# Kernel optimization log

Hardware: AMD Instinct MI355X
Metric: run time of the kernel (lower is better)

The kernel has to match this reference:

```python
import jax, jax.numpy as jnp
import numpy as np

B, N, C = 16384, 4, 512
H = 8
HD = C // H
WIN = 2
SCALE = HD ** -0.5
HID = 2048


def _rel_pos_index(w):
    # same construction as the torch buffer, done in numpy (constant)
    coords = np.stack(np.meshgrid(np.arange(w), np.arange(w), indexing='ij'))  # [2,w,w]
    flat = coords.reshape(2, -1)                      # [2, w*w]
    rel = flat[:, :, None] - flat[:, None, :]         # [2, N, N]
    rel = rel.transpose(1, 2, 0).astype(np.int64)     # [N, N, 2]
    rel[:, :, 0] += w - 1
    rel[:, :, 1] += w - 1
    rel[:, :, 0] *= 2 * w - 1
    return rel.sum(-1)                                # [N, N]

REL_IDX = _rel_pos_index(WIN)


def setup_inputs() -> dict:
    key = jax.random.key(0)
    ks = jax.random.split(key, 8)
    s = lambda fan: 1.0 / np.sqrt(fan)
    return {
        'x': jax.random.normal(ks[0], (B, N, C), jnp.float32),
        'ln_g': jnp.ones((C,), jnp.float32),
        'ln_b': jnp.zeros((C,), jnp.float32),
        'qkv_w': jax.random.normal(ks[1], (3 * C, C), jnp.float32) * s(C),
        'proj_w': jax.random.normal(ks[2], (C, C), jnp.float32) * s(C),
        'proj_b': jnp.zeros((C,), jnp.float32),
        'rpb_table': jax.random.normal(ks[3], ((2 * WIN - 1) ** 2, H), jnp.float32) * 0.02,
        'fc1_w': jax.random.normal(ks[4], (HID, C), jnp.float32) * s(C),
        'fc1_b': jnp.zeros((HID,), jnp.float32),
        'fc2_w': jax.random.normal(ks[5], (C, HID), jnp.float32) * s(HID),
        'fc2_b': jnp.zeros((C,), jnp.float32),
    }


def _layernorm(x, g, b, eps=1e-5):
    mu = jnp.mean(x, axis=-1, keepdims=True)
    var = jnp.mean(jnp.square(x - mu), axis=-1, keepdims=True)
    return (x - mu) * jax.lax.rsqrt(var + eps) * g + b


def reference(x, ln_g, ln_b, qkv_w, proj_w, proj_b, rpb_table, fc1_w, fc1_b, fc2_w, fc2_b):
    # --- attention branch (pre-norm, shared LayerNorm params) ---
    h = _layernorm(x, ln_g, ln_b)
    qkv = h @ qkv_w.T                                  # [B,N,3C]
    qkv = qkv.reshape(B, N, 3, H, HD).transpose(2, 0, 3, 1, 4)  # [3,B,H,N,HD]
    q, k, v = qkv[0], qkv[1], qkv[2]
    attn = jnp.einsum('bhnd,bhmd->bhnm', q, k) * SCALE  # [B,H,N,N]
    bias = rpb_table[REL_IDX.reshape(-1)].reshape(N, N, H).transpose(2, 0, 1)  # [H,N,N]
    attn = jax.nn.softmax(attn + bias[None], axis=-1)
    o = jnp.einsum('bhnm,bhmd->bhnd', attn, v)          # [B,H,N,HD]
    o = o.transpose(0, 2, 1, 3).reshape(B, N, C)
    o = o @ proj_w.T + proj_b
    x = x + o
    # --- MLP branch (same LayerNorm params reused, as in the torch code) ---
    h = _layernorm(x, ln_g, ln_b)
    h = jax.nn.gelu(h @ fc1_w.T + fc1_b, approximate=False)
    h = h @ fc2_w.T + fc2_b
    return x + h
```

## Files before the change

kernel.cpp:

```cpp
#include <hip/hip_runtime.h>
#include <hip/hip_bf16.h>
#include <math.h>

#define BQ   16384
#define CH   512
#define NH   8
#define HID  2048
#define NTOK (BQ*4)

using bf16 = __hip_bfloat16;
typedef __bf16 bf16x8 __attribute__((ext_vector_type(8)));
typedef float  f32x4  __attribute__((ext_vector_type(4)));

#define FENCE() asm volatile("" ::: "memory")

__device__ __forceinline__ void gload16(const void* g, void* l) {
    __builtin_amdgcn_global_load_lds(
        (const __attribute__((address_space(1))) void*)g,
        (__attribute__((address_space(3))) void*)l, 16, 0, 0);
}

__global__ __launch_bounds__(256) void packw(const float* __restrict__ Wsrc,
                                             bf16* __restrict__ out, int N, int K) {
    int q = blockIdx.x * 256 + threadIdx.x;
    int NSk = K >> 5;
    int total = (N >> 7) * NSk * 512;
    if (q >= total) return;
    int l  = q & 63;
    int jj = (q >> 6) & 1;
    int w  = (q >> 7) & 3;
    int s  = (q >> 9) % NSk;
    int cb = q / (NSk * 512);
    int row = cb * 128 + w * 32 + jj * 16 + (l >> 2);
    int k   = s * 32 + ((l & 3) ^ ((l >> 3) & 3)) * 8;
    const float* src = Wsrc + (size_t)row * K + k;
    float4 v0 = *(const float4*)src;
    float4 v1 = *(const float4*)(src + 4);
    __align__(16) bf16 t[8];
    t[0] = __float2bfloat16(v0.x); t[1] = __float2bfloat16(v0.y);
    t[2] = __float2bfloat16(v0.z); t[3] = __float2bfloat16(v0.w);
    t[4] = __float2bfloat16(v1.x); t[5] = __float2bfloat16(v1.y);
    t[6] = __float2bfloat16(v1.z); t[7] = __float2bfloat16(v1.w);
    *(uint4*)&out[(size_t)q * 8] = *(const uint4*)t;
}

__global__ __launch_bounds__(256) void ln_kernel(const float* __restrict__ x,
                                                 const float* __restrict__ g,
                                                 const float* __restrict__ b,
                                                 bf16* __restrict__ out) {
    int row  = blockIdx.x * 4 + (threadIdx.x >> 6);
    int lane = threadIdx.x & 63;
    const float* xr = x + (size_t)row * CH;
    int c0 = lane * 8;
    float4 v0 = *(const float4*)&xr[c0];
    float4 v1 = *(const float4*)&xr[c0 + 4];
    float s  = v0.x + v0.y + v0.z + v0.w + v1.x + v1.y + v1.z + v1.w;
    float sq = v0.x*v0.x + v0.y*v0.y + v0.z*v0.z + v0.w*v0.w
             + v1.x*v1.x + v1.y*v1.y + v1.z*v1.z + v1.w*v1.w;
#pragma unroll
    for (int off = 32; off >= 1; off >>= 1) {
        s  += __shfl_xor(s,  off, 64);
        sq += __shfl_xor(sq, off, 64);
    }
    float mu  = s * (1.0f / CH);
    float var = sq * (1.0f / CH) - mu * mu;
    float rs  = rsqrtf(var + 1e-5f);
    float4 g0 = *(const float4*)&g[c0];
    float4 g1 = *(const float4*)&g[c0 + 4];
    float4 b0 = *(const float4*)&b[c0];
    float4 b1 = *(const float4*)&b[c0 + 4];
    __align__(16) bf16 t[8];
    t[0] = __float2bfloat16((v0.x - mu) * rs * g0.x + b0.x);
    t[1] = __float2bfloat16((v0.y - mu) * rs * g0.y + b0.y);
    t[2] = __float2bfloat16((v0.z - mu) * rs * g0.z + b0.z);
    t[3] = __float2bfloat16((v0.w - mu) * rs * g0.w + b0.w);
    t[4] = __float2bfloat16((v1.x - mu) * rs * g1.x + b1.x);
    t[5] = __float2bfloat16((v1.y - mu) * rs * g1.y + b1.y);
    t[6] = __float2bfloat16((v1.z - mu) * rs * g1.z + b1.z);
    t[7] = __float2bfloat16((v1.w - mu) * rs * g1.w + b1.w);
    *(uint4*)&out[(size_t)row * CH + c0] = *(const uint4*)t;
}

template<int EPI>
__global__ __launch_bounds__(512, 4)
void gemm256x128(const bf16* __restrict__ A, const bf16* __restrict__ Bp,
                 int M, int N, int K, int nbx,
                 const float* __restrict__ bias,
                 const float* resid, float* outF, bf16* __restrict__ outB) {
    __shared__ __align__(16) char lds[49152];
    const int tid  = threadIdx.x;
    const int w    = tid >> 6;
    const int lane = tid & 63;

    const int nb  = gridDim.x;
    const int id  = blockIdx.x;
    const int swz = (id & 7) * (nb >> 3) + (id >> 3);
    const int bx  = swz % nbx, by = swz / nbx;
    const int bm = by * 256, bn = bx * 128;
    const int wrq = w >> 1;
    const int wch = w & 1;
    const int NSk = K >> 5;

    const int rl  = lane >> 2;
    const int kpe = ((lane & 3) ^ ((lane >> 3) & 3)) * 8;
    const bf16* gA0 = A + (size_t)(bm + w * 32 + rl) * K + kpe;
    const bf16* gA1 = gA0 + (size_t)16 * K;
    const bf16* gB = Bp + (size_t)(bn >> 7) * NSk * 4096 + w * 512 + lane * 8;

    const int kslot = ((lane >> 4) ^ ((lane >> 1) & 3));
    const int aoff = (wrq * 64 + (lane & 15)) * 64 + kslot * 16;
    const int boff = 16384 + (wch * 64 + (lane & 15)) * 64 + kslot * 16;

    f32x4 acc[4][4] = {};

    auto stage = [&](int s) {
        char* base = (char*)lds + (s & 1) * 24576;
        gload16(gA0 + (size_t)s * 32, base + w * 2048);
        gload16(gA1 + (size_t)s * 32, base + w * 2048 + 1024);
        gload16(gB  + (size_t)s * 4096, base + 16384 + w * 1024);
    };

    auto compute = [&](int slot) {
        const char* base = (const char*)lds + slot * 24576;
        bf16x8 av[4], bv[4];
#pragma unroll
        for (int n = 0; n < 4; ++n)
            bv[n] = *(const bf16x8*)(base + boff + n * 1024);
#pragma unroll
        for (int m = 0; m < 4; ++m)
            av[m] = *(const bf16x8*)(base + aoff + m * 1024);
#pragma unroll
        for (int m = 0; m < 4; ++m)
#pragma unroll
            for (int n = 0; n < 4; ++n)
                acc[m][n] = __builtin_amdgcn_mfma_f32_16x16x32_bf16(av[m], bv[n], acc[m][n], 0, 0, 0);
    };

#define WAITV(n) asm volatile("s_waitcnt vmcnt(" #n ")" ::: "memory")

    stage(0);
    for (int s = 0; s < NSk - 1; ++s) {
        stage(s + 1);
        WAITV(3);
        __builtin_amdgcn_s_barrier();
        FENCE();
        compute(s & 1);
        FENCE();
        __builtin_amdgcn_s_barrier();
    }
    WAITV(0);
    __builtin_amdgcn_s_barrier();
    FENCE();
    compute((NSk - 1) & 1);
#undef WAITV

    const int erow0 = bm + wrq * 64 + (lane >> 4) * 4;
    const int ecol0 = bn + wch * 64 + (lane & 15);
#pragma unroll
    for (int m = 0; m < 4; ++m) {
#pragma unroll
        for (int n = 0; n < 4; ++n) {
            int col = ecol0 + n * 16;
#pragma unroll
            for (int r = 0; r < 4; ++r) {
                int row = erow0 + m * 16 + r;
                size_t idx = (size_t)row * N + col;
                float v = acc[m][n][r];
                if (EPI == 0) {
                    outB[idx] = __float2bfloat16(v);
                } else if (EPI == 1) {
                    outF[idx] = v + bias[col] + resid[idx];
                } else {
                    float t = v + bias[col];
                    float u2 = 1.5957691216f * t * (1.0f + 0.044715f * t * t);
                    float e = __expf(u2);
                    float r = __builtin_amdgcn_rcpf(e + 1.0f);
                    outB[idx] = __float2bfloat16(t - t * r);
                }
            }
        }
    }
}

__global__ __launch_bounds__(256)
void attn_kernel(const bf16* __restrict__ qkv, const float* __restrict__ rpb,
                 bf16* __restrict__ o) {
    __shared__ __align__(16) bf16 sT[4 * 1536];
    __shared__ float sS[NH][4][4];
    __shared__ float sP[NH][4][4];
    int b   = blockIdx.x;
    int tid = threadIdx.x;
    const bf16* src = qkv + (size_t)b * (4 * 1536);
#pragma unroll
    for (int it = 0; it < 3; ++it) {
        int e = (it * 256 + tid) * 8;
        *(uint4*)&sT[e] = *(const uint4*)&src[e];
    }
    __syncthreads();
    if (tid < 128) {
        int h = tid >> 4, i = (tid >> 2) & 3, j = tid & 3;
        const bf16* q = &sT[i * 1536 + h * 64];
        const bf16* k = &sT[j * 1536 + 512 + h * 64];
        float acc = 0.f;
#pragma unroll
        for (int d = 0; d < 64; ++d)
            acc += __bfloat162float(q[d]) * __bfloat162float(k[d]);
        int rel = (((i >> 1) - (j >> 1)) + 1) * 3 + (((i & 1) - (j & 1)) + 1);
        sS[h][i][j] = acc * 0.125f + rpb[rel * NH + h];
    }
    __syncthreads();
    if (tid < 32) {
        int h = tid >> 2, i = tid & 3;
        float s0 = sS[h][i][0], s1 = sS[h][i][1], s2 = sS[h][i][2], s3 = sS[h][i][3];
        float mx = fmaxf(fmaxf(s0, s1), fmaxf(s2, s3));
        float e0 = expf(s0 - mx), e1 = expf(s1 - mx), e2 = expf(s2 - mx), e3 = expf(s3 - mx);
        float inv = 1.f / (e0 + e1 + e2 + e3);
        sP[h][i][0] = e0 * inv; sP[h][i][1] = e1 * inv;
        sP[h][i][2] = e2 * inv; sP[h][i][3] = e3 * inv;
    }
    __syncthreads();
    {
        int h = tid >> 5, tl = tid & 31;
        int d = tl * 2;
        const bf16* v = &sT[1024 + h * 64 + d];
#pragma unroll
        for (int i = 0; i < 4; ++i) {
            float p0 = sP[h][i][0], p1 = sP[h][i][1], p2 = sP[h][i][2], p3 = sP[h][i][3];
            float o0 = p0 * __bfloat162float(v[0])        + p1 * __bfloat162float(v[1536])
                     + p2 * __bfloat162float(v[2 * 1536]) + p3 * __bfloat162float(v[3 * 1536]);
            float o1 = p0 * __bfloat162float(v[1])            + p1 * __bfloat162float(v[1536 + 1])
                     + p2 * __bfloat162float(v[2 * 1536 + 1]) + p3 * __bfloat162float(v[3 * 1536 + 1]);
            __hip_bfloat162 pr;
            pr.x = __float2bfloat16(o0);
            pr.y = __float2bfloat16(o1);
            *(__hip_bfloat162*)&o[(size_t)(b * 4 + i) * CH + h * 64 + d] = pr;
        }
    }
}

extern "C" void kernel_launch(void* const* d_in, const int* in_sizes, int n_in,
                              void* d_out, int out_size, void* d_ws, size_t ws_size,
                              hipStream_t stream) {
    const float* x      = (const float*)d_in[0];
    const float* ln_g   = (const float*)d_in[1];
    const float* ln_b   = (const float*)d_in[2];
    const float* qkv_w  = (const float*)d_in[3];
    const float* proj_w = (const float*)d_in[4];
    const float* proj_b = (const float*)d_in[5];
    const float* rpb    = (const float*)d_in[6];
    const float* fc1_w  = (const float*)d_in[7];
    const float* fc1_b  = (const float*)d_in[8];
    const float* fc2_w  = (const float*)d_in[9];
    const float* fc2_b  = (const float*)d_in[10];
    float* out = (float*)d_out;

    char* ws = (char*)d_ws;
    bf16* wQKV  = (bf16*)ws;  ws += (size_t)1536 * 512 * 2;
    bf16* wPROJ = (bf16*)ws;  ws += (size_t)512  * 512 * 2;
    bf16* wFC1  = (bf16*)ws;  ws += (size_t)2048 * 512 * 2;
    bf16* wFC2  = (bf16*)ws;  ws += (size_t)512 * 2048 * 2;
    bf16* hA    = (bf16*)ws;  ws += (size_t)NTOK * 512 * 2;
    bf16* big   = (bf16*)ws;
    const size_t needed = 6291456ull + 67108864ull + 268435456ull;
    if (ws_size < needed) return;

    packw<<<384, 256, 0, stream>>>(qkv_w,  wQKV, 1536, 512);
    packw<<<128, 256, 0, stream>>>(proj_w, wPROJ, 512, 512);
    packw<<<512, 256, 0, stream>>>(fc1_w,  wFC1, 2048, 512);
    packw<<<512, 256, 0, stream>>>(fc2_w,  wFC2, 512, 2048);

    ln_kernel<<<NTOK / 4, 256, 0, stream>>>(x, ln_g, ln_b, hA);
    gemm256x128<0><<<dim3(256 * 12), 512, 0, stream>>>(
        hA, wQKV, NTOK, 1536, 512, 12, nullptr, nullptr, nullptr, big);
    attn_kernel<<<BQ, 256, 0, stream>>>(big, rpb, hA);
    gemm256x128<1><<<dim3(256 * 4), 512, 0, stream>>>(
        hA, wPROJ, NTOK, 512, 512, 4, proj_b, x, out, nullptr);
    ln_kernel<<<NTOK / 4, 256, 0, stream>>>(out, ln_g, ln_b, hA);
    gemm256x128<2><<<dim3(256 * 16), 512, 0, stream>>>(
        hA, wFC1, NTOK, 2048, 512, 16, fc1_b, nullptr, nullptr, big);
    gemm256x128<1><<<dim3(256 * 4), 512, 0, stream>>>(
        big, wFC2, NTOK, 512, 2048, 4, fc2_b, out, out, nullptr);
}
```

Measured before the change: 769.7 us.

## Store attention residual in bf16 and merge weight packing into one launch

```diff
diff --git a/kernel.cpp b/kernel.cpp
--- a/kernel.cpp
+++ b/kernel.cpp
@@ -20,12 +20,8 @@
         (__attribute__((address_space(3))) void*)l, 16, 0, 0);
 }
 
-__global__ __launch_bounds__(256) void packw(const float* __restrict__ Wsrc,
-                                             bf16* __restrict__ out, int N, int K) {
-    int q = blockIdx.x * 256 + threadIdx.x;
+__device__ __forceinline__ void packw_one(const float* Wsrc, bf16* out, int q, int K) {
     int NSk = K >> 5;
-    int total = (N >> 7) * NSk * 512;
-    if (q >= total) return;
     int l  = q & 63;
     int jj = (q >> 6) & 1;
     int w  = (q >> 7) & 3;
@@ -44,19 +40,42 @@
     *(uint4*)&out[(size_t)q * 8] = *(const uint4*)t;
 }
 
-__global__ __launch_bounds__(256) void ln_kernel(const float* __restrict__ x,
+__global__ __launch_bounds__(256)
+void packall(const float* qkv_w, const float* proj_w,
+             const float* fc1_w, const float* fc2_w,
+             bf16* wQKV, bf16* wPROJ, bf16* wFC1, bf16* wFC2) {
+    int q = blockIdx.x * 256 + threadIdx.x;
+    if (q < 98304)            packw_one(qkv_w,  wQKV,  q,           512);
+    else if (q < 131072)      packw_one(proj_w, wPROJ, q - 98304,   512);
+    else if (q < 262144)      packw_one(fc1_w,  wFC1,  q - 131072,  512);
+    else                      packw_one(fc2_w,  wFC2,  q - 262144, 2048);
+}
+
+template<int BF16IN>
+__global__ __launch_bounds__(256) void ln_kernel(const void* __restrict__ xin,
                                                  const float* __restrict__ g,
                                                  const float* __restrict__ b,
                                                  bf16* __restrict__ out) {
     int row  = blockIdx.x * 4 + (threadIdx.x >> 6);
     int lane = threadIdx.x & 63;
-    const float* xr = x + (size_t)row * CH;
     int c0 = lane * 8;
-    float4 v0 = *(const float4*)&xr[c0];
-    float4 v1 = *(const float4*)&xr[c0 + 4];
-    float s  = v0.x + v0.y + v0.z + v0.w + v1.x + v1.y + v1.z + v1.w;
-    float sq = v0.x*v0.x + v0.y*v0.y + v0.z*v0.z + v0.w*v0.w
-             + v1.x*v1.x + v1.y*v1.y + v1.z*v1.z + v1.w*v1.w;
+    float f[8];
+    if (BF16IN) {
+        const bf16* xr = (const bf16*)xin + (size_t)row * CH;
+        union { uint4 u4; bf16 h[8]; } uu;
+        uu.u4 = *(const uint4*)&xr[c0];
+#pragma unroll
+        for (int i = 0; i < 8; ++i) f[i] = __bfloat162float(uu.h[i]);
+    } else {
+        const float* xr = (const float*)xin + (size_t)row * CH;
+        float4 v0 = *(const float4*)&xr[c0];
+        float4 v1 = *(const float4*)&xr[c0 + 4];
+        f[0]=v0.x; f[1]=v0.y; f[2]=v0.z; f[3]=v0.w;
+        f[4]=v1.x; f[5]=v1.y; f[6]=v1.z; f[7]=v1.w;
+    }
+    float s = 0.f, sq = 0.f;
+#pragma unroll
+    for (int i = 0; i < 8; ++i) { s += f[i]; sq += f[i] * f[i]; }
 #pragma unroll
     for (int off = 32; off >= 1; off >>= 1) {
         s  += __shfl_xor(s,  off, 64);
@@ -69,15 +88,12 @@
     float4 g1 = *(const float4*)&g[c0 + 4];
     float4 b0 = *(const float4*)&b[c0];
     float4 b1 = *(const float4*)&b[c0 + 4];
+    float gg[8] = {g0.x,g0.y,g0.z,g0.w,g1.x,g1.y,g1.z,g1.w};
+    float bb[8] = {b0.x,b0.y,b0.z,b0.w,b1.x,b1.y,b1.z,b1.w};
     __align__(16) bf16 t[8];
-    t[0] = __float2bfloat16((v0.x - mu) * rs * g0.x + b0.x);
-    t[1] = __float2bfloat16((v0.y - mu) * rs * g0.y + b0.y);
-    t[2] = __float2bfloat16((v0.z - mu) * rs * g0.z + b0.z);
-    t[3] = __float2bfloat16((v0.w - mu) * rs * g0.w + b0.w);
-    t[4] = __float2bfloat16((v1.x - mu) * rs * g1.x + b1.x);
-    t[5] = __float2bfloat16((v1.y - mu) * rs * g1.y + b1.y);
-    t[6] = __float2bfloat16((v1.z - mu) * rs * g1.z + b1.z);
-    t[7] = __float2bfloat16((v1.w - mu) * rs * g1.w + b1.w);
+#pragma unroll
+    for (int i = 0; i < 8; ++i)
+        t[i] = __float2bfloat16((f[i] - mu) * rs * gg[i] + bb[i]);
     *(uint4*)&out[(size_t)row * CH + c0] = *(const uint4*)t;
 }
 
@@ -86,7 +102,8 @@
 void gemm256x128(const bf16* __restrict__ A, const bf16* __restrict__ Bp,
                  int M, int N, int K, int nbx,
                  const float* __restrict__ bias,
-                 const float* resid, float* outF, bf16* __restrict__ outB) {
+                 const float* residF, const bf16* residB,
+                 float* outF, bf16* __restrict__ outB) {
     __shared__ __align__(16) char lds[49152];
     const int tid  = threadIdx.x;
     const int w    = tid >> 6;
@@ -169,13 +186,17 @@
                 if (EPI == 0) {
                     outB[idx] = __float2bfloat16(v);
                 } else if (EPI == 1) {
-                    outF[idx] = v + bias[col] + resid[idx];
-                } else {
+                    outF[idx] = v + bias[col] + residF[idx];
+                } else if (EPI == 2) {
                     float t = v + bias[col];
                     float u2 = 1.5957691216f * t * (1.0f + 0.044715f * t * t);
                     float e = __expf(u2);
-                    float r = __builtin_amdgcn_rcpf(e + 1.0f);
-                    outB[idx] = __float2bfloat16(t - t * r);
+                    float rcp = __builtin_amdgcn_rcpf(e + 1.0f);
+                    outB[idx] = __float2bfloat16(t - t * rcp);
+                } else if (EPI == 3) {
+                    outB[idx] = __float2bfloat16(v + bias[col] + residF[idx]);
+                } else {
+                    outF[idx] = v + bias[col] + __bfloat162float(residB[idx]);
                 }
             }
         }
@@ -260,24 +281,36 @@
     bf16* wFC1  = (bf16*)ws;  ws += (size_t)2048 * 512 * 2;
     bf16* wFC2  = (bf16*)ws;  ws += (size_t)512 * 2048 * 2;
     bf16* hA    = (bf16*)ws;  ws += (size_t)NTOK * 512 * 2;
-    bf16* big   = (bf16*)ws;
-    const size_t needed = 6291456ull + 67108864ull + 268435456ull;
+    bf16* big   = (bf16*)ws;  ws += (size_t)NTOK * 2048 * 2;
+    bf16* x1b   = (bf16*)ws;
+    const size_t needed  = 6291456ull + 67108864ull + 268435456ull;
+    const size_t needed2 = needed + 67108864ull;
     if (ws_size < needed) return;
-
-    packw<<<384, 256, 0, stream>>>(qkv_w,  wQKV, 1536, 512);
-    packw<<<128, 256, 0, stream>>>(proj_w, wPROJ, 512, 512);
-    packw<<<512, 256, 0, stream>>>(fc1_w,  wFC1, 2048, 512);
-    packw<<<512, 256, 0, stream>>>(fc2_w,  wFC2, 512, 2048);
-
-    ln_kernel<<<NTOK / 4, 256, 0, stream>>>(x, ln_g, ln_b, hA);
+    const bool useb = (ws_size >= needed2);
+
+    packall<<<1536, 256, 0, stream>>>(qkv_w, proj_w, fc1_w, fc2_w,
+                                      wQKV, wPROJ, wFC1, wFC2);
+
+    ln_kernel<0><<<NTOK / 4, 256, 0, stream>>>(x, ln_g, ln_b, hA);
     gemm256x128<0><<<dim3(256 * 12), 512, 0, stream>>>(
-        hA, wQKV, NTOK, 1536, 512, 12, nullptr, nullptr, nullptr, big);
+        hA, wQKV, NTOK, 1536, 512, 12, nullptr, nullptr, nullptr, nullptr, big);
     attn_kernel<<<BQ, 256, 0, stream>>>(big, rpb, hA);
-    gemm256x128<1><<<dim3(256 * 4), 512, 0, stream>>>(
-        hA, wPROJ, NTOK, 512, 512, 4, proj_b, x, out, nullptr);
-    ln_kernel<<<NTOK / 4, 256, 0, stream>>>(out, ln_g, ln_b, hA);
-    gemm256x128<2><<<dim3(256 * 16), 512, 0, stream>>>(
-        hA, wFC1, NTOK, 2048, 512, 16, fc1_b, nullptr, nullptr, big);
-    gemm256x128<1><<<dim3(256 * 4), 512, 0, stream>>>(
-        big, wFC2, NTOK, 512, 2048, 4, fc2_b, out, out, nullptr);
-}
+
+    if (useb) {
+        gemm256x128<3><<<dim3(256 * 4), 512, 0, stream>>>(
+            hA, wPROJ, NTOK, 512, 512, 4, proj_b, x, nullptr, nullptr, x1b);
+        ln_kernel<1><<<NTOK / 4, 256, 0, stream>>>(x1b, ln_g, ln_b, hA);
+        gemm256x128<2><<<dim3(256 * 16), 512, 0, stream>>>(
+            hA, wFC1, NTOK, 2048, 512, 16, fc1_b, nullptr, nullptr, nullptr, big);
+        gemm256x128<4><<<dim3(256 * 4), 512, 0, stream>>>(
+            big, wFC2, NTOK, 512, 2048, 4, fc2_b, nullptr, x1b, out, nullptr);
+    } else {
+        gemm256x128<1><<<dim3(256 * 4), 512, 0, stream>>>(
+            hA, wPROJ, NTOK, 512, 512, 4, proj_b, x, nullptr, out, nullptr);
+        ln_kernel<0><<<NTOK / 4, 256, 0, stream>>>(out, ln_g, ln_b, hA);
+        gemm256x128<2><<<dim3(256 * 16), 512, 0, stream>>>(
+            hA, wFC1, NTOK, 2048, 512, 16, fc1_b, nullptr, nullptr, nullptr, big);
+        gemm256x128<1><<<dim3(256 * 4), 512, 0, stream>>>(
+            big, wFC2, NTOK, 512, 2048, 4, fc2_b, out, nullptr, out, nullptr);
+    }
+}
```

After: 738.7 us. 4.0% less time.
